# Kernel tuning notes

Hardware: AMD Instinct MI355X
Metric: run time of the kernel (lower is better)

The kernel has to match this reference:

```python
import jax, jax.numpy as jnp
import numpy as np

C = 128
EPS = 1e-5

def setup_inputs() -> dict:
    key = jax.random.key(0)
    ks = jax.random.split(key, 12)
    B, D, H, W = 2, 16, 16, 16
    inp = jax.random.normal(ks[0], (B, C, D, H, W), dtype=jnp.float32)
    s = 1.0 / np.sqrt(C)
    return {
        "inp": inp,
        "gamma": jnp.ones((C,), jnp.float32),
        "beta": jnp.zeros((C,), jnp.float32),
        "Wq": jax.random.normal(ks[1], (C, C), jnp.float32) * s,
        "bq": jnp.zeros((C,), jnp.float32),
        "Wk": jax.random.normal(ks[2], (C, C), jnp.float32) * s,
        "bk": jnp.zeros((C,), jnp.float32),
        "Wv": jax.random.normal(ks[3], (C, C), jnp.float32) * s,
        "bv": jnp.zeros((C,), jnp.float32),
        "Wo": jax.random.normal(ks[4], (C, C), jnp.float32) * s,
        "bo": jnp.zeros((C,), jnp.float32),
    }

def reference(inp, gamma, beta, Wq, bq, Wk, bk, Wv, bv, Wo, bo):
    B, ch, D, H, W = inp.shape
    N = D * H * W
    x = inp.reshape(B, ch, N)  # (B,C,N)
    # BatchNorm3d (training-mode batch stats, biased variance, affine)
    mean = jnp.mean(x, axis=(0, 2))
    var = jnp.var(x, axis=(0, 2))
    hn = (x - mean[None, :, None]) * jax.lax.rsqrt(var + EPS)[None, :, None]
    hn = hn * gamma[None, :, None] + beta[None, :, None]
    # 1x1 Conv3d == per-voxel channel mixing
    q = jnp.einsum('oc,bcn->bon', Wq, hn) + bq[None, :, None]
    k = jnp.einsum('oc,bcn->bon', Wk, hn) + bk[None, :, None]
    v = jnp.einsum('oc,bcn->bon', Wv, hn) + bv[None, :, None]
    scale = 1.0 / jnp.sqrt(jnp.asarray(ch, q.dtype))
    # attn[b,i,j] = softmax_j( q_i . k_j / sqrt(C) )
    attn = jax.nn.softmax(jnp.einsum('bci,bcj->bij', q, k) * scale, axis=-1)
    # out[b,c,i] = sum_j v[b,c,j] * attn[b,i,j]
    h = jnp.einsum('bcj,bij->bci', v, attn)
    h = jnp.einsum('oc,bcn->bon', Wo, h) + bo[None, :, None]
    return inp + h.reshape(B, ch, D, H, W)
```

## Files before the change

kernel.cpp:

```cpp
#include <hip/hip_runtime.h>

#define C 128
#define NSP 4096
#define BB 2
#define EPS 1e-5f

typedef float f32x4 __attribute__((ext_vector_type(4)));
typedef __bf16 bf16x8 __attribute__((ext_vector_type(8)));
typedef __bf16 bf16x4 __attribute__((ext_vector_type(4)));

__device__ __forceinline__ float b2f(__bf16 x) { return (float)x; }
__device__ __forceinline__ __bf16 f2b(float x) { return (__bf16)x; }

__device__ __forceinline__ float fexp2(float x) {
#if __has_builtin(__builtin_amdgcn_exp2f)
    return __builtin_amdgcn_exp2f(x);
#else
    return exp2f(x);
#endif
}

__device__ __forceinline__ bool is_bf(const void* gamma) {
    return *(const unsigned int*)gamma == 0x3F803F80u;
}
__device__ __forceinline__ float ldf(const void* p, size_t i, bool bf) {
    return bf ? (float)((const __bf16*)p)[i] : ((const float*)p)[i];
}
struct F8 { float v[8]; };
__device__ __forceinline__ F8 ld8(const void* p, size_t i, bool bf) {
    F8 r;
    if (bf) {
        bf16x8 t = *(const bf16x8*)((const __bf16*)p + i);
#pragma unroll
        for (int k = 0; k < 8; k++) r.v[k] = (float)t[k];
    } else {
        const float4* q = (const float4*)((const float*)p + i);
        float4 a = q[0], b = q[1];
        r.v[0]=a.x; r.v[1]=a.y; r.v[2]=a.z; r.v[3]=a.w;
        r.v[4]=b.x; r.v[5]=b.y; r.v[6]=b.z; r.v[7]=b.w;
    }
    return r;
}
struct F4 { float v[4]; };
__device__ __forceinline__ F4 ld4(const void* p, size_t i, bool bf) {
    F4 r;
    if (bf) {
        bf16x4 t = *(const bf16x4*)((const __bf16*)p + i);
#pragma unroll
        for (int k = 0; k < 4; k++) r.v[k] = (float)t[k];
    } else {
        float4 t = *(const float4*)((const float*)p + i);
        r.v[0]=t.x; r.v[1]=t.y; r.v[2]=t.z; r.v[3]=t.w;
    }
    return r;
}

__device__ __forceinline__ void cp16(const void* g, void* l) {
    __builtin_amdgcn_global_load_lds(
        (const __attribute__((address_space(1))) unsigned int*)g,
        (__attribute__((address_space(3))) unsigned int*)l, 16, 0, 0);
}

__global__ void k_stats(const void* __restrict__ x, const void* __restrict__ gamma,
                        float* __restrict__ meanv, float* __restrict__ rstd) {
    bool bf = is_bf(gamma);
    int c = blockIdx.x;
    int tid = threadIdx.x;
    float s = 0.f, ss = 0.f;
#pragma unroll
    for (int it = 0; it < 4; it++) {
        int flat = tid + it * 256;
        int half = flat >> 9;
        size_t off = ((size_t)(half * C + c)) * NSP + (size_t)(flat & 511) * 8;
        F8 v = ld8(x, off, bf);
#pragma unroll
        for (int k = 0; k < 8; k++) { s += v.v[k]; ss += v.v[k] * v.v[k]; }
    }
    for (int d = 32; d; d >>= 1) { s += __shfl_down(s, d); ss += __shfl_down(ss, d); }
    __shared__ float sh[8];
    int wv = tid >> 6, ln = tid & 63;
    if (ln == 0) { sh[wv] = s; sh[4 + wv] = ss; }
    __syncthreads();
    if (tid == 0) {
        float S = sh[0] + sh[1] + sh[2] + sh[3];
        float SS = sh[4] + sh[5] + sh[6] + sh[7];
        float m = S / (float)(BB * NSP);
        float v = SS / (float)(BB * NSP) - m * m;
        meanv[c] = m;
        rstd[c] = rsqrtf(fmaxf(v, 0.f) + EPS);
    }
}

__global__ void k_fold(const void* __restrict__ Wq, const void* __restrict__ bq,
                       const void* __restrict__ Wk, const void* __restrict__ bk,
                       const void* __restrict__ Wv, const void* __restrict__ bv,
                       const void* __restrict__ gamma, const void* __restrict__ beta,
                       const float* __restrict__ meanv, const float* __restrict__ rstd,
                       __bf16* __restrict__ Wp, float* __restrict__ bp) {
    bool bfm = is_bf(gamma);
    int o = blockIdx.x;
    int m = blockIdx.y;
    int c = threadIdx.x;
    const void* W  = (m == 0) ? Wq : ((m == 1) ? Wk : Wv);
    const void* bi = (m == 0) ? bq : ((m == 1) ? bk : bv);
    float scl = (m == 0) ? (0.08838834764831845f * 1.4426950408889634f) : 1.0f;
    float w = ldf(W, (size_t)o * C + c, bfm);
    float g = ldf(gamma, c, bfm) * rstd[c];
    Wp[((size_t)m * C + o) * C + c] = f2b(w * g * scl);
    float contrib = w * (ldf(beta, c, bfm) - g * meanv[c]);
    for (int d = 32; d; d >>= 1) contrib += __shfl_down(contrib, d);
    __shared__ float sh[2];
    if ((c & 63) == 0) sh[c >> 6] = contrib;
    __syncthreads();
    if (c == 0) bp[m * C + o] = (ldf(bi, o, bfm) + sh[0] + sh[1]) * scl;
}

__global__ void k_qkv(const void* __restrict__ x, const __bf16* __restrict__ Wp,
                      const float* __restrict__ bp, const void* __restrict__ gamma,
                      __bf16* __restrict__ Qt, __bf16* __restrict__ Kt,
                      __bf16* __restrict__ Vn) {
    bool bf = is_bf(gamma);
    __shared__ __attribute__((aligned(16))) __bf16 wsh[C * 136];
    __shared__ __attribute__((aligned(16))) __bf16 xsh[C * 72];
    __shared__ float bsh[C];
    int b = blockIdx.z, m = blockIdx.y, nt = blockIdx.x * 64;
    int tid = threadIdx.x;
    const __bf16* W = Wp + (size_t)m * C * C;
#pragma unroll
    for (int it = 0; it < 8; it++) {
        int flat = tid + it * 256;
        int o = flat >> 4, c0 = (flat & 15) * 8;
        *(bf16x8*)(wsh + o * 136 + c0) = *(const bf16x8*)(W + (size_t)o * C + c0);
    }
    size_t xbase = (size_t)b * C * NSP;
#pragma unroll
    for (int it = 0; it < 4; it++) {
        int flat = tid + it * 256;
        int c = flat >> 3, nc = (flat & 7) * 8;
        F8 v = ld8(x, xbase + (size_t)c * NSP + nt + nc, bf);
        bf16x8 tv;
#pragma unroll
        for (int k = 0; k < 8; k++) tv[k] = f2b(v.v[k]);
        *(bf16x8*)(xsh + c * 72 + nc) = tv;
    }
    if (tid < C) bsh[tid] = bp[m * C + tid];
    __syncthreads();

    int o0 = (tid >> 4) * 8;
    int n0 = (tid & 15) * 4;
    float acc[8][4];
#pragma unroll
    for (int i = 0; i < 8; i++) {
        float bias = bsh[o0 + i];
#pragma unroll
        for (int k = 0; k < 4; k++) acc[i][k] = bias;
    }
    for (int c = 0; c < C; c += 4) {
        float xf[4][4];
#pragma unroll
        for (int cc = 0; cc < 4; cc++) {
            bf16x4 x4 = *(const bf16x4*)(xsh + (c + cc) * 72 + n0);
#pragma unroll
            for (int k = 0; k < 4; k++) xf[cc][k] = b2f(x4[k]);
        }
#pragma unroll
        for (int i = 0; i < 8; i++) {
            bf16x4 w4 = *(const bf16x4*)(wsh + (o0 + i) * 136 + c);
#pragma unroll
            for (int cc = 0; cc < 4; cc++) {
                float wf = b2f(w4[cc]);
#pragma unroll
                for (int k = 0; k < 4; k++) acc[i][k] += wf * xf[cc][k];
            }
        }
    }
    if (m < 2) {
        __bf16* base = ((m == 0) ? Qt : Kt) + ((size_t)b * NSP + nt + n0) * C + o0;
#pragma unroll
        for (int k = 0; k < 4; k++) {
            bf16x8 tv;
#pragma unroll
            for (int i = 0; i < 8; i++) tv[i] = f2b(acc[i][k]);
            *(bf16x8*)(base + (size_t)k * C) = tv;
        }
    } else {
#pragma unroll
        for (int i = 0; i < 8; i++) {
            bf16x4 tv;
#pragma unroll
            for (int k = 0; k < 4; k++) tv[k] = f2b(acc[i][k]);
            *(bf16x4*)(Vn + ((size_t)b * C + o0 + i) * NSP + nt + n0) = tv;
        }
    }
}

#define KT_OFF(buf) ((buf) * 32768)
#define VT_OFF(buf) (65536 + (buf) * 32768)
#define PT_OFF      131072
#define LSH_OFF     139264

__launch_bounds__(512, 2)
__global__ void k_attn(const __bf16* __restrict__ Qt, const __bf16* __restrict__ Kt,
                       const __bf16* __restrict__ Vn, const void* __restrict__ gamma,
                       void* __restrict__ Oc ) {
    extern __shared__ char smem[];
    __bf16* pt = (__bf16*)(smem + PT_OFF);
    float* lsh = (float*)(smem + LSH_OFF);

    bool bf = is_bf(gamma);
    int id = blockIdx.x;
    int xcd = id & 7;
    int b = xcd >> 2;
    int qt = (xcd & 3) * 32 + (id >> 3);
    int tid = threadIdx.x;
    int w = tid >> 6, lane = tid & 63, quad = lane >> 4, l15 = lane & 15;
    int s = w & 3, h = w >> 2;

    const __bf16* kb = Kt + (size_t)b * NSP * C;
    const __bf16* vb = Vn + (size_t)b * C * NSP;

    bf16x8 qreg[2][4];
#pragma unroll
    for (int it2 = 0; it2 < 2; it2++)
#pragma unroll
        for (int ks = 0; ks < 4; ks++)
            qreg[it2][ks] = *(const bf16x8*)(Qt + ((size_t)b * NSP + qt * 32 + it2 * 16 + l15) * C + ks * 32 + quad * 8);

    auto stageK = [&](int tile, int buf) {
        __bf16* kt = (__bf16*)(smem + KT_OFF(buf));
#pragma unroll
        for (int c4 = 0; c4 < 4; c4++) {
            int ch = w * 4 + c4;
            int jl = ch * 4 + (lane >> 4);
            int p = lane & 15;
            int cb = p ^ (jl & 15);
            cp16(kb + ((size_t)(tile * 128 + jl)) * C + cb * 8, kt + ch * 512);
        }
    };
    auto stageV = [&](int tile, int buf) {
        __bf16* vt = (__bf16*)(smem + VT_OFF(buf));
#pragma unroll
        for (int c4 = 0; c4 < 4; c4++) {
            int ch = w * 4 + c4;
            int cl = ch * 4 + (lane >> 4);
            int p = lane & 15;
            int jc = p ^ (cl & 15);
            cp16(vb + (size_t)cl * NSP + tile * 128 + jc * 8, vt + ch * 512);
        }
    };

    f32x4 o_acc[4][2];
#pragma unroll
    for (int cb2 = 0; cb2 < 4; cb2++)
#pragma unroll
        for (int it2 = 0; it2 < 2; it2++)
            o_acc[cb2][it2] = (f32x4){0.f, 0.f, 0.f, 0.f};
    float l_acc[2] = {0.f, 0.f};

    stageK(0, 0); stageV(0, 0);

#pragma unroll 2
    for (int it = 0; it < 32; it++) {
        int cur = it & 1, nxt = cur ^ 1;
        const __bf16* ktc = (const __bf16*)(smem + KT_OFF(cur));
        const __bf16* vtc = (const __bf16*)(smem + VT_OFF(cur));
        asm volatile("s_waitcnt vmcnt(4) lgkmcnt(0)\n\ts_barrier" ::: "memory");
        if (it < 31) stageK(it + 1, nxt);
        f32x4 sacc[2];
        sacc[0] = (f32x4){0.f, 0.f, 0.f, 0.f};
        sacc[1] = (f32x4){0.f, 0.f, 0.f, 0.f};
#pragma unroll
        for (int ks = 0; ks < 4; ks++) {
            bf16x8 kf = *(const bf16x8*)(ktc + (w * 16 + l15) * 128 + (((ks * 4 + quad) ^ l15) * 8));
            sacc[0] = __builtin_amdgcn_mfma_f32_16x16x32_bf16(kf, qreg[0][ks], sacc[0], 0, 0, 0);
            sacc[1] = __builtin_amdgcn_mfma_f32_16x16x32_bf16(kf, qreg[1][ks], sacc[1], 0, 0, 0);
        }
#pragma unroll
        for (int it2 = 0; it2 < 2; it2++) {
            bf16x4 p4;
#pragma unroll
            for (int r = 0; r < 4; r++) {
                float p = fexp2(sacc[it2][r]);
                l_acc[it2] += p;
                p4[r] = f2b(p);
            }
            int i = it2 * 16 + l15;
            int cc = 2 * w + (quad >> 1);
            *(bf16x4*)(pt + i * 128 + ((cc ^ (i & 7)) * 8) + (quad & 1) * 4) = p4;
        }
        if (it < 31) {
            asm volatile("s_waitcnt vmcnt(4) lgkmcnt(0)\n\ts_barrier" ::: "memory");
            stageV(it + 1, nxt);
        } else {
            asm volatile("s_waitcnt vmcnt(0) lgkmcnt(0)\n\ts_barrier" ::: "memory");
        }
        bf16x8 pfr[2];
#pragma unroll
        for (int it2 = 0; it2 < 2; it2++) {
            int i = it2 * 16 + l15;
            pfr[it2] = *(const bf16x8*)(pt + i * 128 + (((s * 4 + quad) ^ (i & 7)) * 8));
        }
#pragma unroll
        for (int cblk = 0; cblk < 4; cblk++) {
            bf16x8 vf = *(const bf16x8*)(vtc + (h * 64 + cblk * 16 + l15) * 128 + (((s * 4 + quad) ^ l15) * 8));
            o_acc[cblk][0] = __builtin_amdgcn_mfma_f32_16x16x32_bf16(vf, pfr[0], o_acc[cblk][0], 0, 0, 0);
            o_acc[cblk][1] = __builtin_amdgcn_mfma_f32_16x16x32_bf16(vf, pfr[1], o_acc[cblk][1], 0, 0, 0);
        }
    }

#pragma unroll
    for (int it2 = 0; it2 < 2; it2++) {
        l_acc[it2] += __shfl_xor(l_acc[it2], 16);
        l_acc[it2] += __shfl_xor(l_acc[it2], 32);
    }
    if (lane < 16) { lsh[w * 32 + lane] = l_acc[0]; lsh[w * 32 + 16 + lane] = l_acc[1]; }
    float* arrf = (float*)smem;
#pragma unroll
    for (int cblk = 0; cblk < 4; cblk++)
#pragma unroll
        for (int it2 = 0; it2 < 2; it2++)
#pragma unroll
            for (int r = 0; r < 4; r++)
                arrf[(s * 128 + h * 64 + cblk * 16 + quad * 4 + r) * 37 + it2 * 16 + l15] = o_acc[cblk][it2][r];
    __syncthreads();
    if (tid < 32) {
        float ls = 0.f;
#pragma unroll
        for (int w8 = 0; w8 < 8; w8++) ls += lsh[w8 * 32 + tid];
        lsh[256 + tid] = 1.0f / ls;
    }
    __syncthreads();
    int c = tid >> 2, i0 = (tid & 3) * 8;
    float val[8];
#pragma unroll
    for (int k = 0; k < 8; k++) {
        int i = i0 + k;
        float v = arrf[(0 * 128 + c) * 37 + i] + arrf[(1 * 128 + c) * 37 + i]
                + arrf[(2 * 128 + c) * 37 + i] + arrf[(3 * 128 + c) * 37 + i];
        val[k] = v * lsh[256 + i];
    }
    size_t addr = ((size_t)b * C + c) * NSP + qt * 32 + i0;
    if (bf) {
        bf16x8 tv;
#pragma unroll
        for (int k = 0; k < 8; k++) tv[k] = f2b(val[k]);
        *(bf16x8*)((__bf16*)Oc + addr) = tv;
    } else {
        float4 t0, t1;
        t0.x = val[0]; t0.y = val[1]; t0.z = val[2]; t0.w = val[3];
        t1.x = val[4]; t1.y = val[5]; t1.z = val[6]; t1.w = val[7];
        *(float4*)((float*)Oc + addr) = t0;
        *(float4*)((float*)Oc + addr + 4) = t1;
    }
}

__global__ void k_proj(const void* __restrict__ Wo, const void* __restrict__ bo,
                       const void* __restrict__ inp, const void* __restrict__ gamma,
                       void* __restrict__ out) {
    bool bf = is_bf(gamma);
    __shared__ __attribute__((aligned(16))) __bf16 wsh[C * 136];
    __shared__ __attribute__((aligned(16))) float hsh[C * 36];
    __shared__ float bsh[C];
    int b = blockIdx.y, nt = blockIdx.x * 32;
    int tid = threadIdx.x;
#pragma unroll
    for (int it = 0; it < 8; it++) {
        int flat = tid + it * 256;
        int o = flat >> 4, c0 = (flat & 15) * 8;
        F8 v = ld8(Wo, (size_t)o * C + c0, bf);
        bf16x8 tv;
#pragma unroll
        for (int k = 0; k < 8; k++) tv[k] = f2b(v.v[k]);
        *(bf16x8*)(wsh + o * 136 + c0) = tv;
    }
#pragma unroll
    for (int it = 0; it < 4; it++) {
        int flat = tid + it * 256;
        int c = flat >> 3, nc = (flat & 7) * 4;
        F4 v = ld4(out, ((size_t)b * C + c) * NSP + nt + nc, bf);
        float4 tv; tv.x = v.v[0]; tv.y = v.v[1]; tv.z = v.v[2]; tv.w = v.v[3];
        *(float4*)(hsh + c * 36 + nc) = tv;
    }
    if (tid < C) bsh[tid] = ldf(bo, tid, bf);
    __syncthreads();

    int o0 = (tid >> 4) * 8;
    int n0 = (tid & 15) * 2;
    float acc[8][2];
#pragma unroll
    for (int i = 0; i < 8; i++) { acc[i][0] = 0.f; acc[i][1] = 0.f; }
    for (int c = 0; c < C; c += 4) {
        float xf[4][2];
#pragma unroll
        for (int cc = 0; cc < 4; cc++) {
            xf[cc][0] = hsh[(c + cc) * 36 + n0];
            xf[cc][1] = hsh[(c + cc) * 36 + n0 + 1];
        }
#pragma unroll
        for (int i = 0; i < 8; i++) {
            bf16x4 w4 = *(const bf16x4*)(wsh + (o0 + i) * 136 + c);
#pragma unroll
            for (int cc = 0; cc < 4; cc++) {
                float wf = b2f(w4[cc]);
                acc[i][0] += wf * xf[cc][0];
                acc[i][1] += wf * xf[cc][1];
            }
        }
    }
#pragma unroll
    for (int i = 0; i < 8; i++) {
        float bias = bsh[o0 + i];
        size_t addr = ((size_t)b * C + o0 + i) * NSP + nt + n0;
#pragma unroll
        for (int k = 0; k < 2; k++) {
            float val = acc[i][k] + bias + ldf(inp, addr + k, bf);
            if (bf) ((__bf16*)out)[addr + k] = f2b(val);
            else    ((float*)out)[addr + k] = val;
        }
    }
}

extern "C" void kernel_launch(void* const* d_in, const int* in_sizes, int n_in,
                              void* d_out, int out_size, void* d_ws, size_t ws_size,
                              hipStream_t stream) {
    const void* inp   = d_in[0];
    const void* gamma = d_in[1];
    const void* beta  = d_in[2];
    const void* Wq    = d_in[3];
    const void* bq    = d_in[4];
    const void* Wk    = d_in[5];
    const void* bk    = d_in[6];
    const void* Wv    = d_in[7];
    const void* bv    = d_in[8];
    const void* Wo    = d_in[9];
    const void* bo    = d_in[10];

    char* ws = (char*)d_ws;
    float* meanv = (float*)(ws + 0);
    float* rstd  = (float*)(ws + 512);
    float* bp    = (float*)(ws + 1024);
    __bf16* Wp = (__bf16*)(ws + 4096);
    __bf16* Qt = (__bf16*)(ws + 131072);
    __bf16* Kt = (__bf16*)(ws + 2228224);
    __bf16* Vn = (__bf16*)(ws + 4325376);

    (void)hipFuncSetAttribute((const void*)k_attn,
                              hipFuncAttributeMaxDynamicSharedMemorySize, 140416);

    k_stats<<<dim3(C), dim3(256), 0, stream>>>(inp, gamma, meanv, rstd);
    k_fold<<<dim3(C, 3), dim3(C), 0, stream>>>(Wq, bq, Wk, bk, Wv, bv, gamma, beta, meanv, rstd, Wp, bp);
    k_qkv<<<dim3(64, 3, 2), dim3(256), 0, stream>>>(inp, Wp, bp, gamma, Qt, Kt, Vn);
    k_attn<<<dim3(256), dim3(512), 140416, stream>>>(Qt, Kt, Vn, gamma, d_out);
    k_proj<<<dim3(128, 2), dim3(256), 0, stream>>>(Wo, bo, inp, gamma, d_out);
}
```

Before: 148.0 us.

## Double attention query tile to 64 rows per block, halving grid size

```diff
diff --git a/kernel.cpp b/kernel.cpp
--- a/kernel.cpp
+++ b/kernel.cpp
@@ -197,7 +197,7 @@
 #define KT_OFF(buf) ((buf) * 32768)
 #define VT_OFF(buf) (65536 + (buf) * 32768)
 #define PT_OFF      131072
-#define LSH_OFF     139264
+#define LSH_OFF     147456
 
 __launch_bounds__(512, 2)
 __global__ void k_attn(const __bf16* __restrict__ Qt, const __bf16* __restrict__ Kt,
@@ -211,7 +211,7 @@
     int id = blockIdx.x;
     int xcd = id & 7;
     int b = xcd >> 2;
-    int qt = (xcd & 3) * 32 + (id >> 3);
+    int qg = (xcd & 3) * 16 + (id >> 3);
     int tid = threadIdx.x;
     int w = tid >> 6, lane = tid & 63, quad = lane >> 4, l15 = lane & 15;
     int s = w & 3, h = w >> 2;
@@ -219,12 +219,12 @@
     const __bf16* kb = Kt + (size_t)b * NSP * C;
     const __bf16* vb = Vn + (size_t)b * C * NSP;
 
-    bf16x8 qreg[2][4];
-#pragma unroll
-    for (int it2 = 0; it2 < 2; it2++)
+    bf16x8 qreg[4][4];
+#pragma unroll
+    for (int it2 = 0; it2 < 4; it2++)
 #pragma unroll
         for (int ks = 0; ks < 4; ks++)
-            qreg[it2][ks] = *(const bf16x8*)(Qt + ((size_t)b * NSP + qt * 32 + it2 * 16 + l15) * C + ks * 32 + quad * 8);
+            qreg[it2][ks] = *(const bf16x8*)(Qt + ((size_t)b * NSP + qg * 64 + it2 * 16 + l15) * C + ks * 32 + quad * 8);
 
     auto stageK = [&](int tile, int buf) {
         __bf16* kt = (__bf16*)(smem + KT_OFF(buf));
@@ -249,34 +249,35 @@
         }
     };
 
-    f32x4 o_acc[4][2];
+    f32x4 o_acc[4][4];
 #pragma unroll
     for (int cb2 = 0; cb2 < 4; cb2++)
 #pragma unroll
-        for (int it2 = 0; it2 < 2; it2++)
+        for (int it2 = 0; it2 < 4; it2++)
             o_acc[cb2][it2] = (f32x4){0.f, 0.f, 0.f, 0.f};
-    float l_acc[2] = {0.f, 0.f};
+    float l_acc[4] = {0.f, 0.f, 0.f, 0.f};
 
     stageK(0, 0); stageV(0, 0);
 
-#pragma unroll 2
     for (int it = 0; it < 32; it++) {
         int cur = it & 1, nxt = cur ^ 1;
         const __bf16* ktc = (const __bf16*)(smem + KT_OFF(cur));
         const __bf16* vtc = (const __bf16*)(smem + VT_OFF(cur));
         asm volatile("s_waitcnt vmcnt(4) lgkmcnt(0)\n\ts_barrier" ::: "memory");
         if (it < 31) stageK(it + 1, nxt);
-        f32x4 sacc[2];
-        sacc[0] = (f32x4){0.f, 0.f, 0.f, 0.f};
-        sacc[1] = (f32x4){0.f, 0.f, 0.f, 0.f};
+        f32x4 sacc[4];
+#pragma unroll
+        for (int it2 = 0; it2 < 4; it2++) sacc[it2] = (f32x4){0.f, 0.f, 0.f, 0.f};
 #pragma unroll
         for (int ks = 0; ks < 4; ks++) {
             bf16x8 kf = *(const bf16x8*)(ktc + (w * 16 + l15) * 128 + (((ks * 4 + quad) ^ l15) * 8));
             sacc[0] = __builtin_amdgcn_mfma_f32_16x16x32_bf16(kf, qreg[0][ks], sacc[0], 0, 0, 0);
             sacc[1] = __builtin_amdgcn_mfma_f32_16x16x32_bf16(kf, qreg[1][ks], sacc[1], 0, 0, 0);
-        }
-#pragma unroll
-        for (int it2 = 0; it2 < 2; it2++) {
+            sacc[2] = __builtin_amdgcn_mfma_f32_16x16x32_bf16(kf, qreg[2][ks], sacc[2], 0, 0, 0);
+            sacc[3] = __builtin_amdgcn_mfma_f32_16x16x32_bf16(kf, qreg[3][ks], sacc[3], 0, 0, 0);
+        }
+#pragma unroll
+        for (int it2 = 0; it2 < 4; it2++) {
             bf16x4 p4;
 #pragma unroll
             for (int r = 0; r < 4; r++) {
@@ -294,9 +295,9 @@
         } else {
             asm volatile("s_waitcnt vmcnt(0) lgkmcnt(0)\n\ts_barrier" ::: "memory");
         }
-        bf16x8 pfr[2];
-#pragma unroll
-        for (int it2 = 0; it2 < 2; it2++) {
+        bf16x8 pfr[4];
+#pragma unroll
+        for (int it2 = 0; it2 < 4; it2++) {
             int i = it2 * 16 + l15;
             pfr[it2] = *(const bf16x8*)(pt + i * 128 + (((s * 4 + quad) ^ (i & 7)) * 8));
         }
@@ -305,52 +306,63 @@
             bf16x8 vf = *(const bf16x8*)(vtc + (h * 64 + cblk * 16 + l15) * 128 + (((s * 4 + quad) ^ l15) * 8));
             o_acc[cblk][0] = __builtin_amdgcn_mfma_f32_16x16x32_bf16(vf, pfr[0], o_acc[cblk][0], 0, 0, 0);
             o_acc[cblk][1] = __builtin_amdgcn_mfma_f32_16x16x32_bf16(vf, pfr[1], o_acc[cblk][1], 0, 0, 0);
-        }
-    }
-
-#pragma unroll
-    for (int it2 = 0; it2 < 2; it2++) {
+            o_acc[cblk][2] = __builtin_amdgcn_mfma_f32_16x16x32_bf16(vf, pfr[2], o_acc[cblk][2], 0, 0, 0);
+            o_acc[cblk][3] = __builtin_amdgcn_mfma_f32_16x16x32_bf16(vf, pfr[3], o_acc[cblk][3], 0, 0, 0);
+        }
+    }
+
+#pragma unroll
+    for (int it2 = 0; it2 < 4; it2++) {
         l_acc[it2] += __shfl_xor(l_acc[it2], 16);
         l_acc[it2] += __shfl_xor(l_acc[it2], 32);
     }
-    if (lane < 16) { lsh[w * 32 + lane] = l_acc[0]; lsh[w * 32 + 16 + lane] = l_acc[1]; }
+    __syncthreads();
+    if (lane < 16) {
+#pragma unroll
+        for (int it2 = 0; it2 < 4; it2++) lsh[w * 64 + it2 * 16 + lane] = l_acc[it2];
+    }
     float* arrf = (float*)smem;
 #pragma unroll
     for (int cblk = 0; cblk < 4; cblk++)
 #pragma unroll
-        for (int it2 = 0; it2 < 2; it2++)
+        for (int it2 = 0; it2 < 4; it2++)
 #pragma unroll
             for (int r = 0; r < 4; r++)
-                arrf[(s * 128 + h * 64 + cblk * 16 + quad * 4 + r) * 37 + it2 * 16 + l15] = o_acc[cblk][it2][r];
-    __syncthreads();
-    if (tid < 32) {
+                arrf[(s * 128 + h * 64 + cblk * 16 + quad * 4 + r) * 68 + it2 * 16 + l15] = o_acc[cblk][it2][r];
+    __syncthreads();
+    if (tid < 64) {
         float ls = 0.f;
 #pragma unroll
-        for (int w8 = 0; w8 < 8; w8++) ls += lsh[w8 * 32 + tid];
-        lsh[256 + tid] = 1.0f / ls;
-    }
-    __syncthreads();
-    int c = tid >> 2, i0 = (tid & 3) * 8;
-    float val[8];
-#pragma unroll
-    for (int k = 0; k < 8; k++) {
+        for (int w8 = 0; w8 < 8; w8++) ls += lsh[w8 * 64 + tid];
+        lsh[512 + tid] = 1.0f / ls;
+    }
+    __syncthreads();
+    int c = tid >> 2, i0 = (tid & 3) * 16;
+    float val[16];
+#pragma unroll
+    for (int k = 0; k < 16; k++) {
         int i = i0 + k;
-        float v = arrf[(0 * 128 + c) * 37 + i] + arrf[(1 * 128 + c) * 37 + i]
-                + arrf[(2 * 128 + c) * 37 + i] + arrf[(3 * 128 + c) * 37 + i];
-        val[k] = v * lsh[256 + i];
-    }
-    size_t addr = ((size_t)b * C + c) * NSP + qt * 32 + i0;
+        float v = arrf[(0 * 128 + c) * 68 + i] + arrf[(1 * 128 + c) * 68 + i]
+                + arrf[(2 * 128 + c) * 68 + i] + arrf[(3 * 128 + c) * 68 + i];
+        val[k] = v * lsh[512 + i];
+    }
+    size_t addr = ((size_t)b * C + c) * NSP + qg * 64 + i0;
     if (bf) {
-        bf16x8 tv;
-#pragma unroll
-        for (int k = 0; k < 8; k++) tv[k] = f2b(val[k]);
-        *(bf16x8*)((__bf16*)Oc + addr) = tv;
+#pragma unroll
+        for (int v8 = 0; v8 < 2; v8++) {
+            bf16x8 tv;
+#pragma unroll
+            for (int k = 0; k < 8; k++) tv[k] = f2b(val[v8 * 8 + k]);
+            *(bf16x8*)((__bf16*)Oc + addr + v8 * 8) = tv;
+        }
     } else {
-        float4 t0, t1;
-        t0.x = val[0]; t0.y = val[1]; t0.z = val[2]; t0.w = val[3];
-        t1.x = val[4]; t1.y = val[5]; t1.z = val[6]; t1.w = val[7];
-        *(float4*)((float*)Oc + addr) = t0;
-        *(float4*)((float*)Oc + addr + 4) = t1;
+#pragma unroll
+        for (int v4 = 0; v4 < 4; v4++) {
+            float4 t;
+            t.x = val[v4 * 4 + 0]; t.y = val[v4 * 4 + 1];
+            t.z = val[v4 * 4 + 2]; t.w = val[v4 * 4 + 3];
+            *(float4*)((float*)Oc + addr + v4 * 4) = t;
+        }
     }
 }
 
@@ -445,11 +457,11 @@
     __bf16* Vn = (__bf16*)(ws + 4325376);
 
     (void)hipFuncSetAttribute((const void*)k_attn,
-                              hipFuncAttributeMaxDynamicSharedMemorySize, 140416);
+                              hipFuncAttributeMaxDynamicSharedMemorySize, 149760);
 
     k_stats<<<dim3(C), dim3(256), 0, stream>>>(inp, gamma, meanv, rstd);
     k_fold<<<dim3(C, 3), dim3(C), 0, stream>>>(Wq, bq, Wk, bk, Wv, bv, gamma, beta, meanv, rstd, Wp, bp);
     k_qkv<<<dim3(64, 3, 2), dim3(256), 0, stream>>>(inp, Wp, bp, gamma, Qt, Kt, Vn);
-    k_attn<<<dim3(256), dim3(512), 140416, stream>>>(Qt, Kt, Vn, gamma, d_out);
+    k_attn<<<dim3(128), dim3(512), 149760, stream>>>(Qt, Kt, Vn, gamma, d_out);
     k_proj<<<dim3(128, 2), dim3(256), 0, stream>>>(Wo, bo, inp, gamma, d_out);
 }
```

Result: slower. 167.5 us (+13.1%).
